# Kernel tuning notes

Measured on AMD Instinct MI355X. Metric: run time of the kernel, lower is better.

Reference implementation:

```python
import jax, jax.numpy as jnp
import numpy as np
import math

MODEL_DIM = 512
NUM_HEADS = 8
FFN_DIM = 2048
LN_EPS = 1e-5


def setup_inputs() -> dict:
    key = jax.random.key(0)
    ks = jax.random.split(key, 16)
    B, S, D, F = 1, 4096, MODEL_DIM, FFN_DIM
    s = 1.0 / math.sqrt(D)
    inp = {
        "x": jax.random.normal(ks[0], (B, S, D), dtype=jnp.float32),
        # Linear weights stored [in, out] (transpose of torch's [out, in]); y = x @ W + b
        "wq": jax.random.normal(ks[1], (D, D), dtype=jnp.float32) * s,
        "bq": jnp.zeros((D,), dtype=jnp.float32),
        "wk": jax.random.normal(ks[2], (D, D), dtype=jnp.float32) * s,
        "bk": jnp.zeros((D,), dtype=jnp.float32),
        "wv": jax.random.normal(ks[3], (D, D), dtype=jnp.float32) * s,
        "bv": jnp.zeros((D,), dtype=jnp.float32),
        "wo": jax.random.normal(ks[4], (D, D), dtype=jnp.float32) * s,
        "bo": jnp.zeros((D,), dtype=jnp.float32),
        "w1": jax.random.normal(ks[5], (D, F), dtype=jnp.float32) * s,
        "b1": jnp.zeros((F,), dtype=jnp.float32),
        "w2": jax.random.normal(ks[6], (F, D), dtype=jnp.float32) * (1.0 / math.sqrt(F)),
        "b2": jnp.zeros((D,), dtype=jnp.float32),
        "gamma": jnp.ones((D,), dtype=jnp.float32),
        "beta": jnp.zeros((D,), dtype=jnp.float32),
    }
    return inp


def _layer_norm(x, gamma, beta):
    mu = jnp.mean(x, axis=-1, keepdims=True)
    var = jnp.mean(jnp.square(x - mu), axis=-1, keepdims=True)
    return (x - mu) * jax.lax.rsqrt(var + LN_EPS) * gamma + beta


def reference(x, wq, bq, wk, bk, wv, bv, wo, bo, w1, b1, w2, b2, gamma, beta):
    B, S, D = x.shape
    H = NUM_HEADS
    dph = D // H
    q = x @ wq + bq
    k = x @ wk + bk
    v = x @ wv + bv
    # Faithful to original: direct view [B,S,D] -> [B*H, S, dph] (no head transpose)
    q = q.reshape(B * H, S, dph)
    k = k.reshape(B * H, S, dph)
    v = v.reshape(B * H, S, dph)
    scores = jnp.einsum('bqd,bkd->bqk', q, k) / math.sqrt(dph)  # [B*H, S, S]
    attn = jax.nn.softmax(scores, axis=-1)
    context = jnp.einsum('bqk,bkd->bqd', attn, v).reshape(B, S, D)
    attn_out = context @ wo + bo + x  # residual (dropout is identity in eval)
    ffn = jax.nn.relu(attn_out @ w1 + b1) @ w2 + b2
    out = _layer_norm(ffn + attn_out, gamma, beta)
    return out, attn
```

## Files before the change

### kernel.cpp

```cpp
#include <hip/hip_runtime.h>
#include <hip/hip_bf16.h>
#include <cstdint>
#include <cstddef>

#define SEQ 4096
#define DM  512
#define NH  8
#define DPH 64
#define FF  2048

using short8 = __attribute__((ext_vector_type(8))) short;
using f32x4  = __attribute__((ext_vector_type(4))) float;

__device__ inline float b2f(unsigned short u) {
    union { unsigned int i; float f; } c; c.i = ((unsigned int)u) << 16; return c.f;
}
__device__ inline unsigned short f2b(float f) {
    union { float f; unsigned int u; } c; c.f = f;
    unsigned int u = c.u;
    return (unsigned short)((u + 0x7fffu + ((u >> 16) & 1u)) >> 16);
}

template<int AF32>
__global__ __launch_bounds__(256) void gemm_kernel(
    const void* __restrict__ Av, const unsigned short* __restrict__ BT,
    const float* __restrict__ bias, const unsigned short* __restrict__ res,
    unsigned short* __restrict__ Cb, float* __restrict__ Cf,
    int M, int N, int K, long sA, long sB, long sC, float scale, int relu)
{
    const long z = blockIdx.z;
    BT += z * sB;
    const long co = z * sC;

    const int lane = threadIdx.x & 63;
    const int wid  = threadIdx.x >> 6;
    const int quad = lane >> 4;
    const int col  = lane & 15;
    const int m0 = blockIdx.y * 64 + wid * 16;
    const int n0 = blockIdx.x * 64;

    f32x4 acc[4];
    const f32x4 zero4 = {0.f, 0.f, 0.f, 0.f};
#pragma unroll
    for (int t = 0; t < 4; ++t) acc[t] = zero4;

    const unsigned short* arow16 = nullptr;
    const float*          arow32 = nullptr;
    if (AF32) arow32 = (const float*)Av          + z * sA + (size_t)(m0 + col) * K + quad * 8;
    else      arow16 = (const unsigned short*)Av + z * sA + (size_t)(m0 + col) * K + quad * 8;
    const unsigned short* brow = BT + (size_t)(n0 + col) * K + quad * 8;

    for (int k0 = 0; k0 < K; k0 += 32) {
        short8 a;
        if (AF32) {
            const float4 f0 = *(const float4*)(arow32 + k0);
            const float4 f1 = *(const float4*)(arow32 + k0 + 4);
            a[0] = (short)f2b(f0.x); a[1] = (short)f2b(f0.y);
            a[2] = (short)f2b(f0.z); a[3] = (short)f2b(f0.w);
            a[4] = (short)f2b(f1.x); a[5] = (short)f2b(f1.y);
            a[6] = (short)f2b(f1.z); a[7] = (short)f2b(f1.w);
        } else {
            a = *(const short8*)(arow16 + k0);
        }
#pragma unroll
        for (int t = 0; t < 4; ++t) {
            short8 b = *(const short8*)(brow + (size_t)t * 16 * K + k0);
            acc[t] = __builtin_amdgcn_mfma_f32_16x16x32_bf16(a, b, acc[t], 0, 0, 0);
        }
    }

#pragma unroll
    for (int t = 0; t < 4; ++t) {
        const int n = n0 + t * 16 + col;
        const float bv = bias ? bias[n] : 0.f;
#pragma unroll
        for (int r = 0; r < 4; ++r) {
            const int row = m0 + quad * 4 + r;
            float v = acc[t][r] * scale + bv;
            const size_t idx = (size_t)row * N + n;
            if (res)  v += b2f(res[idx]);
            if (relu) v = fmaxf(v, 0.f);
            if (Cf) Cf[co + idx] = v;
            else    Cb[co + idx] = f2b(v);
        }
    }
}

__global__ __launch_bounds__(256) void transpose_cast_kernel(
    const float* __restrict__ src, unsigned short* __restrict__ dst, int R, int C)
{
    __shared__ float tile[32][33];
    const int c0 = blockIdx.x * 32, r0 = blockIdx.y * 32;
    const int tx = threadIdx.x & 31, ty = threadIdx.x >> 5;
#pragma unroll
    for (int i = 0; i < 4; ++i)
        tile[ty + i * 8][tx] = src[(size_t)(r0 + ty + i * 8) * C + c0 + tx];
    __syncthreads();
#pragma unroll
    for (int i = 0; i < 4; ++i)
        dst[(size_t)(c0 + ty + i * 8) * R + r0 + tx] = f2b(tile[tx][ty + i * 8]);
}

__global__ __launch_bounds__(256) void transpose_kernel(
    const unsigned short* __restrict__ src, unsigned short* __restrict__ dst,
    int R, int C)
{
    __shared__ unsigned short tile[32][33];
    const long off = (long)blockIdx.z * (long)R * (long)C;
    src += off; dst += off;
    const int c0 = blockIdx.x * 32, r0 = blockIdx.y * 32;
    const int tx = threadIdx.x & 31, ty = threadIdx.x >> 5;
#pragma unroll
    for (int i = 0; i < 4; ++i)
        tile[ty + i * 8][tx] = src[(size_t)(r0 + ty + i * 8) * C + c0 + tx];
    __syncthreads();
#pragma unroll
    for (int i = 0; i < 4; ++i)
        dst[(size_t)(c0 + ty + i * 8) * R + r0 + tx] = tile[tx][ty + i * 8];
}

__global__ __launch_bounds__(256) void cast_kernel(
    const float* __restrict__ src, unsigned short* __restrict__ dst, int n4)
{
    const int i = blockIdx.x * 256 + threadIdx.x;
    if (i >= n4) return;
    const float4 v = ((const float4*)src)[i];
    union { unsigned short s[4]; unsigned long long u; } p;
    p.s[0] = f2b(v.x); p.s[1] = f2b(v.y); p.s[2] = f2b(v.z); p.s[3] = f2b(v.w);
    ((unsigned long long*)dst)[i] = p.u;
}

__global__ __launch_bounds__(256, 8) void fused_attn_kernel(
    const unsigned short* __restrict__ qb,
    const unsigned short* __restrict__ kb,
    const unsigned short* __restrict__ vT,
    float* __restrict__ att,
    unsigned short* __restrict__ ctx)
{
    __shared__ __align__(16) float Pl[4][16 * 36];
    __shared__ float smM[4][16];
    __shared__ float smS[4][16];
    __shared__ __align__(16) float cbuf[2][16 * 68];

    const int id    = blockIdx.x;
    const int h     = id & 7;
    const int strip = id >> 3;
    const int lane  = threadIdx.x & 63;
    const int w     = threadIdx.x >> 6;
    const int quad  = lane >> 4, col = lane & 15;
    const int m0    = strip * 16;

    const unsigned short* Qh = qb + (size_t)h * SEQ * DPH;
    const unsigned short* Kh = kb + (size_t)h * SEQ * DPH;
    const unsigned short* Vh = vT + (size_t)h * SEQ * DPH;
    float* atth = att + (size_t)h * SEQ * SEQ;
    unsigned short* ctxh = ctx + (size_t)h * SEQ * DPH;

    const unsigned short* qrow = Qh + (size_t)(m0 + col) * DPH + quad * 8;
    const short8 aq0 = *(const short8*)(qrow);
    const short8 aq1 = *(const short8*)(qrow + 32);

    const unsigned short* kbase = Kh + (size_t)(w * 1024 + col) * DPH + quad * 8;
    const float SC = 0.125f;
    const f32x4 zero4 = {0.f, 0.f, 0.f, 0.f};

    float m[4], s[4];
#pragma unroll
    for (int r = 0; r < 4; ++r) { m[r] = -1e30f; s[r] = 0.f; }

#pragma unroll 2
    for (int nt = 0; nt < 64; ++nt) {
        const unsigned short* kr = kbase + (size_t)nt * 16 * DPH;
        const short8 b0 = *(const short8*)(kr);
        const short8 b1 = *(const short8*)(kr + 32);
        f32x4 acc = zero4;
        acc = __builtin_amdgcn_mfma_f32_16x16x32_bf16(aq0, b0, acc, 0, 0, 0);
        acc = __builtin_amdgcn_mfma_f32_16x16x32_bf16(aq1, b1, acc, 0, 0, 0);
#pragma unroll
        for (int r = 0; r < 4; ++r) {
            const float v  = acc[r] * SC;
            const float nm = fmaxf(m[r], v);
            const float e  = __expf(fminf(m[r], v) - nm);
            s[r] = (v > m[r]) ? fmaf(s[r], e, 1.f) : (s[r] + e);
            m[r] = nm;
        }
    }
#pragma unroll
    for (int off = 1; off < 16; off <<= 1) {
#pragma unroll
        for (int r = 0; r < 4; ++r) {
            const float mo = __shfl_xor(m[r], off);
            const float so = __shfl_xor(s[r], off);
            const float nm = fmaxf(m[r], mo);
            s[r] = s[r] * __expf(m[r] - nm) + so * __expf(mo - nm);
            m[r] = nm;
        }
    }
    if (col == 0) {
#pragma unroll
        for (int r = 0; r < 4; ++r) { smM[w][quad * 4 + r] = m[r]; smS[w][quad * 4 + r] = s[r]; }
    }
    __syncthreads();
    float inv[4];
#pragma unroll
    for (int r = 0; r < 4; ++r) {
        const int row = quad * 4 + r;
        float M = smM[0][row], S = smS[0][row];
#pragma unroll
        for (int ww = 1; ww < 4; ++ww) {
            const float mo = smM[ww][row];
            const float so = smS[ww][row];
            const float nm = fmaxf(M, mo);
            S = S * __expf(M - nm) + so * __expf(mo - nm);
            M = nm;
        }
        m[r] = M;
        inv[r] = 1.f / S;
    }

    f32x4 cacc[4];
#pragma unroll
    for (int t = 0; t < 4; ++t) cacc[t] = zero4;

    float* Pw = Pl[w];
    float* abase = atth + (size_t)(m0 + quad * 4) * SEQ + w * 1024 + col;
    for (int pr = 0; pr < 32; ++pr) {
#pragma unroll
        for (int sub = 0; sub < 2; ++sub) {
            const int ntl = pr * 2 + sub;
            const unsigned short* kr = kbase + (size_t)ntl * 16 * DPH;
            const short8 b0 = *(const short8*)(kr);
            const short8 b1 = *(const short8*)(kr + 32);
            f32x4 acc = zero4;
            acc = __builtin_amdgcn_mfma_f32_16x16x32_bf16(aq0, b0, acc, 0, 0, 0);
            acc = __builtin_amdgcn_mfma_f32_16x16x32_bf16(aq1, b1, acc, 0, 0, 0);
            float* arow = abase + ntl * 16;
#pragma unroll
            for (int r = 0; r < 4; ++r) {
                const float p = __expf(fmaf(acc[r], SC, -m[r])) * inv[r];
                arow[(size_t)r * SEQ] = p;
                Pw[(quad * 4 + r) * 36 + sub * 16 + col] = p;
            }
        }
        const float4 pa0 = *(const float4*)(Pw + col * 36 + quad * 8);
        const float4 pa1 = *(const float4*)(Pw + col * 36 + quad * 8 + 4);
        union { unsigned short us[8]; short8 v; } ap;
        ap.us[0] = f2b(pa0.x); ap.us[1] = f2b(pa0.y);
        ap.us[2] = f2b(pa0.z); ap.us[3] = f2b(pa0.w);
        ap.us[4] = f2b(pa1.x); ap.us[5] = f2b(pa1.y);
        ap.us[6] = f2b(pa1.z); ap.us[7] = f2b(pa1.w);

        const int kg = w * 1024 + pr * 32;
        const unsigned short* vb0 = Vh + (size_t)col * SEQ + kg + quad * 8;
#pragma unroll
        for (int t = 0; t < 4; ++t) {
            const short8 bv = *(const short8*)(vb0 + (size_t)t * 16 * SEQ);
            cacc[t] = __builtin_amdgcn_mfma_f32_16x16x32_bf16(ap.v, bv, cacc[t], 0, 0, 0);
        }
    }

    if (w & 1) {
        float* cb = cbuf[w >> 1];
#pragma unroll
        for (int t = 0; t < 4; ++t)
#pragma unroll
            for (int r = 0; r < 4; ++r)
                cb[(quad * 4 + r) * 68 + t * 16 + col] = cacc[t][r];
    }
    __syncthreads();
    if (!(w & 1)) {
        const float* cb = cbuf[w >> 1];
#pragma unroll
        for (int t = 0; t < 4; ++t)
#pragma unroll
            for (int r = 0; r < 4; ++r)
                cacc[t][r] += cb[(quad * 4 + r) * 68 + t * 16 + col];
    }
    __syncthreads();
    if (w == 2) {
#pragma unroll
        for (int t = 0; t < 4; ++t)
#pragma unroll
            for (int r = 0; r < 4; ++r)
                cbuf[0][(quad * 4 + r) * 68 + t * 16 + col] = cacc[t][r];
    }
    __syncthreads();
    if (w == 0) {
#pragma unroll
        for (int t = 0; t < 4; ++t) {
#pragma unroll
            for (int r = 0; r < 4; ++r) {
                const float v = cacc[t][r] + cbuf[0][(quad * 4 + r) * 68 + t * 16 + col];
                ctxh[(size_t)(m0 + quad * 4 + r) * DPH + t * 16 + col] = f2b(v);
            }
        }
    }
}

__global__ __launch_bounds__(256) void ln_kernel(
    const float* __restrict__ pre,
    const float* __restrict__ gamma, const float* __restrict__ beta,
    float* __restrict__ out)
{
    __shared__ float redS[4], redQ[4];
    const float* p = pre + (size_t)blockIdx.x * 512;
    const int t = threadIdx.x;
    const int w = t >> 6, lane = t & 63;

    const float2 xv = *(const float2*)(p + t * 2);
    float s = xv.x + xv.y;
    float q = xv.x * xv.x + xv.y * xv.y;
#pragma unroll
    for (int off = 32; off; off >>= 1) {
        s += __shfl_xor(s, off);
        q += __shfl_xor(q, off);
    }
    if (lane == 0) { redS[w] = s; redQ[w] = q; }
    __syncthreads();
    s = redS[0] + redS[1] + redS[2] + redS[3];
    q = redQ[0] + redQ[1] + redQ[2] + redQ[3];

    const float mu  = s * (1.f / 512.f);
    const float var = q * (1.f / 512.f) - mu * mu;
    const float rs  = rsqrtf(var + 1e-5f);

    const size_t o = (size_t)blockIdx.x * 512 + t * 2;
    out[o]     = (xv.x - mu) * rs * gamma[t * 2]     + beta[t * 2];
    out[o + 1] = (xv.y - mu) * rs * gamma[t * 2 + 1] + beta[t * 2 + 1];
}

extern "C" void kernel_launch(void* const* d_in, const int* in_sizes, int n_in,
                              void* d_out, int out_size, void* d_ws, size_t ws_size,
                              hipStream_t stream)
{
    (void)in_sizes; (void)n_in; (void)out_size; (void)ws_size;

    const float* x     = (const float*)d_in[0];
    const float* wq    = (const float*)d_in[1];
    const float* bq    = (const float*)d_in[2];
    const float* wk    = (const float*)d_in[3];
    const float* bk    = (const float*)d_in[4];
    const float* wv    = (const float*)d_in[5];
    const float* bv    = (const float*)d_in[6];
    const float* wo    = (const float*)d_in[7];
    const float* bo    = (const float*)d_in[8];
    const float* w1    = (const float*)d_in[9];
    const float* b1    = (const float*)d_in[10];
    const float* w2    = (const float*)d_in[11];
    const float* b2    = (const float*)d_in[12];
    const float* gamma = (const float*)d_in[13];
    const float* beta  = (const float*)d_in[14];

    float* out = (float*)d_out;
    float* att = out + (size_t)SEQ * DM;

    char* wsp = (char*)d_ws;
    auto alloc = [&](size_t bytes) {
        char* p = wsp;
        wsp += (bytes + 255) & ~(size_t)255;
        return p;
    };
    unsigned short* wqT  = (unsigned short*)alloc((size_t)DM * DM * 2);
    unsigned short* wkT  = (unsigned short*)alloc((size_t)DM * DM * 2);
    unsigned short* wvT  = (unsigned short*)alloc((size_t)DM * DM * 2);
    unsigned short* woT  = (unsigned short*)alloc((size_t)DM * DM * 2);
    unsigned short* w1T  = (unsigned short*)alloc((size_t)DM * FF * 2);
    unsigned short* w2T  = (unsigned short*)alloc((size_t)FF * DM * 2);
    unsigned short* xb   = (unsigned short*)alloc((size_t)SEQ * DM * 2);
    unsigned short* qb   = (unsigned short*)alloc((size_t)SEQ * DM * 2);
    unsigned short* kb   = (unsigned short*)alloc((size_t)SEQ * DM * 2);
    unsigned short* vb   = (unsigned short*)alloc((size_t)SEQ * DM * 2);
    unsigned short* vT   = (unsigned short*)alloc((size_t)SEQ * DM * 2);
    unsigned short* ctx  = (unsigned short*)alloc((size_t)SEQ * DM * 2);
    unsigned short* aout = (unsigned short*)alloc((size_t)SEQ * DM * 2);
    unsigned short* ffn1 = (unsigned short*)alloc((size_t)SEQ * FF * 2);
    float*          pre  = (float*)alloc((size_t)SEQ * DM * 4);

    const dim3 blk(256);

    cast_kernel<<<dim3((SEQ * DM / 4 + 255) / 256), blk, 0, stream>>>(x, xb, SEQ * DM / 4);

    transpose_cast_kernel<<<dim3(16, 16), blk, 0, stream>>>(wq, wqT, DM, DM);
    transpose_cast_kernel<<<dim3(16, 16), blk, 0, stream>>>(wk, wkT, DM, DM);
    transpose_cast_kernel<<<dim3(16, 16), blk, 0, stream>>>(wv, wvT, DM, DM);
    transpose_cast_kernel<<<dim3(16, 16), blk, 0, stream>>>(wo, woT, DM, DM);
    transpose_cast_kernel<<<dim3(64, 16), blk, 0, stream>>>(w1, w1T, DM, FF);
    transpose_cast_kernel<<<dim3(16, 64), blk, 0, stream>>>(w2, w2T, FF, DM);

    gemm_kernel<0><<<dim3(8, 64, 1), blk, 0, stream>>>(xb, wqT, bq, nullptr, qb, nullptr,
                                                       SEQ, DM, DM, 0, 0, 0, 1.f, 0);
    gemm_kernel<0><<<dim3(8, 64, 1), blk, 0, stream>>>(xb, wkT, bk, nullptr, kb, nullptr,
                                                       SEQ, DM, DM, 0, 0, 0, 1.f, 0);
    gemm_kernel<0><<<dim3(8, 64, 1), blk, 0, stream>>>(xb, wvT, bv, nullptr, vb, nullptr,
                                                       SEQ, DM, DM, 0, 0, 0, 1.f, 0);

    transpose_kernel<<<dim3(2, 128, 8), blk, 0, stream>>>(vb, vT, SEQ, DPH);

    fused_attn_kernel<<<dim3(2048), blk, 0, stream>>>(qb, kb, vT, att, ctx);

    gemm_kernel<0><<<dim3(8, 64, 1), blk, 0, stream>>>(ctx, woT, bo, xb, aout, nullptr,
                                                       SEQ, DM, DM, 0, 0, 0, 1.f, 0);

    gemm_kernel<0><<<dim3(32, 64, 1), blk, 0, stream>>>(aout, w1T, b1, nullptr, ffn1, nullptr,
                                                        SEQ, FF, DM, 0, 0, 0, 1.f, 1);

    gemm_kernel<0><<<dim3(8, 64, 1), blk, 0, stream>>>(ffn1, w2T, b2, aout, nullptr, pre,
                                                       SEQ, DM, FF, 0, 0, 0, 1.f, 0);

    ln_kernel<<<dim3(SEQ), blk, 0, stream>>>(pre, gamma, beta, out);
}
```

Before: 1.165 ms.

## Tile GEMMs through shared memory and coalesce attention-probability stores

Replaces the register-only GEMM, where each wave streamed A and B straight from global memory, with an LDS-tiled kernel. It uses 128xBN block tiles, register prefetch of the next K slice, and 4xNI MFMA sub-tiles per wave, which raises operand reuse. In the attention kernel, the probability matrix is now written to global memory as float4 row chunks read back from the existing LDS staging buffer, instead of scattered scalar column stores. This adds LDS traffic and two barriers per K step, and the larger tiles halve the GEMM grid sizes.

```diff
diff --git a/kernel.cpp b/kernel.cpp
--- a/kernel.cpp
+++ b/kernel.cpp
@@ -21,67 +21,91 @@
     return (unsigned short)((u + 0x7fffu + ((u >> 16) & 1u)) >> 16);
 }
 
-template<int AF32>
-__global__ __launch_bounds__(256) void gemm_kernel(
-    const void* __restrict__ Av, const unsigned short* __restrict__ BT,
+template<int BN, int NI>
+__global__ __launch_bounds__(256) void tgemm_kernel(
+    const unsigned short* __restrict__ A, const unsigned short* __restrict__ BT,
     const float* __restrict__ bias, const unsigned short* __restrict__ res,
     unsigned short* __restrict__ Cb, float* __restrict__ Cf,
-    int M, int N, int K, long sA, long sB, long sC, float scale, int relu)
-{
-    const long z = blockIdx.z;
-    BT += z * sB;
-    const long co = z * sC;
-
-    const int lane = threadIdx.x & 63;
-    const int wid  = threadIdx.x >> 6;
-    const int quad = lane >> 4;
-    const int col  = lane & 15;
-    const int m0 = blockIdx.y * 64 + wid * 16;
-    const int n0 = blockIdx.x * 64;
-
-    f32x4 acc[4];
+    int M, int N, int K, int relu)
+{
+    __shared__ __align__(16) unsigned short As[128 * 40];
+    __shared__ __align__(16) unsigned short Bs[BN * 40];
+
+    const int t    = threadIdx.x;
+    const int lane = t & 63;
+    const int wid  = t >> 6;
+    const int wr   = wid >> 1, wc = wid & 1;
+    const int quad = lane >> 4, cl = lane & 15;
+    const int m0 = blockIdx.y * 128;
+    const int n0 = blockIdx.x * BN;
+
+    const int srow = t >> 2;
+    const int skc  = t & 3;
+
+    const unsigned short* Arow0 = A  + (size_t)(m0 + srow) * K + skc * 8;
+    const unsigned short* Arow1 = Arow0 + (size_t)64 * K;
+    const unsigned short* Brow0 = BT + (size_t)(n0 + srow) * K + skc * 8;
+    const unsigned short* Brow1 = Brow0 + (size_t)64 * K;
+
+    f32x4 acc[4][NI];
     const f32x4 zero4 = {0.f, 0.f, 0.f, 0.f};
 #pragma unroll
-    for (int t = 0; t < 4; ++t) acc[t] = zero4;
-
-    const unsigned short* arow16 = nullptr;
-    const float*          arow32 = nullptr;
-    if (AF32) arow32 = (const float*)Av          + z * sA + (size_t)(m0 + col) * K + quad * 8;
-    else      arow16 = (const unsigned short*)Av + z * sA + (size_t)(m0 + col) * K + quad * 8;
-    const unsigned short* brow = BT + (size_t)(n0 + col) * K + quad * 8;
+    for (int mi = 0; mi < 4; ++mi)
+#pragma unroll
+        for (int ni = 0; ni < NI; ++ni) acc[mi][ni] = zero4;
+
+    short8 ar0, ar1, br0, br1;
+    ar0 = *(const short8*)(Arow0);
+    ar1 = *(const short8*)(Arow1);
+    br0 = *(const short8*)(Brow0);
+    if constexpr (NI == 4) br1 = *(const short8*)(Brow1);
 
     for (int k0 = 0; k0 < K; k0 += 32) {
-        short8 a;
-        if (AF32) {
-            const float4 f0 = *(const float4*)(arow32 + k0);
-            const float4 f1 = *(const float4*)(arow32 + k0 + 4);
-            a[0] = (short)f2b(f0.x); a[1] = (short)f2b(f0.y);
-            a[2] = (short)f2b(f0.z); a[3] = (short)f2b(f0.w);
-            a[4] = (short)f2b(f1.x); a[5] = (short)f2b(f1.y);
-            a[6] = (short)f2b(f1.z); a[7] = (short)f2b(f1.w);
-        } else {
-            a = *(const short8*)(arow16 + k0);
-        }
-#pragma unroll
-        for (int t = 0; t < 4; ++t) {
-            short8 b = *(const short8*)(brow + (size_t)t * 16 * K + k0);
-            acc[t] = __builtin_amdgcn_mfma_f32_16x16x32_bf16(a, b, acc[t], 0, 0, 0);
-        }
-    }
-
-#pragma unroll
-    for (int t = 0; t < 4; ++t) {
-        const int n = n0 + t * 16 + col;
+        __syncthreads();
+        *(short8*)(&As[srow * 40 + skc * 8])        = ar0;
+        *(short8*)(&As[(srow + 64) * 40 + skc * 8]) = ar1;
+        *(short8*)(&Bs[srow * 40 + skc * 8])        = br0;
+        if constexpr (NI == 4) *(short8*)(&Bs[(srow + 64) * 40 + skc * 8]) = br1;
+        __syncthreads();
+
+        const int kn = k0 + 32;
+        if (kn < K) {
+            ar0 = *(const short8*)(Arow0 + kn);
+            ar1 = *(const short8*)(Arow1 + kn);
+            br0 = *(const short8*)(Brow0 + kn);
+            if constexpr (NI == 4) br1 = *(const short8*)(Brow1 + kn);
+        }
+
+        short8 af[4], bf[NI];
+#pragma unroll
+        for (int mi = 0; mi < 4; ++mi)
+            af[mi] = *(const short8*)(&As[(wr * 64 + mi * 16 + cl) * 40 + quad * 8]);
+#pragma unroll
+        for (int ni = 0; ni < NI; ++ni)
+            bf[ni] = *(const short8*)(&Bs[(wc * (BN / 2) + ni * 16 + cl) * 40 + quad * 8]);
+#pragma unroll
+        for (int mi = 0; mi < 4; ++mi)
+#pragma unroll
+            for (int ni = 0; ni < NI; ++ni)
+                acc[mi][ni] = __builtin_amdgcn_mfma_f32_16x16x32_bf16(af[mi], bf[ni], acc[mi][ni], 0, 0, 0);
+    }
+
+#pragma unroll
+    for (int ni = 0; ni < NI; ++ni) {
+        const int n = n0 + wc * (BN / 2) + ni * 16 + cl;
         const float bv = bias ? bias[n] : 0.f;
 #pragma unroll
-        for (int r = 0; r < 4; ++r) {
-            const int row = m0 + quad * 4 + r;
-            float v = acc[t][r] * scale + bv;
-            const size_t idx = (size_t)row * N + n;
-            if (res)  v += b2f(res[idx]);
-            if (relu) v = fmaxf(v, 0.f);
-            if (Cf) Cf[co + idx] = v;
-            else    Cb[co + idx] = f2b(v);
+        for (int mi = 0; mi < 4; ++mi) {
+#pragma unroll
+            for (int r = 0; r < 4; ++r) {
+                const int row = m0 + wr * 64 + mi * 16 + quad * 4 + r;
+                float v = acc[mi][ni][r] + bv;
+                const size_t idx = (size_t)row * N + n;
+                if (res)  v += b2f(res[idx]);
+                if (relu) v = fmaxf(v, 0.f);
+                if (Cf) Cf[idx] = v;
+                else    Cb[idx] = f2b(v);
+            }
         }
     }
 }
@@ -223,7 +247,9 @@
     for (int t = 0; t < 4; ++t) cacc[t] = zero4;
 
     float* Pw = Pl[w];
-    float* abase = atth + (size_t)(m0 + quad * 4) * SEQ + w * 1024 + col;
+    float* abase = atth + (size_t)m0 * SEQ + w * 1024;
+    const int srow2  = lane >> 3;
+    const int schunk = lane & 7;
     for (int pr = 0; pr < 32; ++pr) {
 #pragma unroll
         for (int sub = 0; sub < 2; ++sub) {
@@ -234,13 +260,17 @@
             f32x4 acc = zero4;
             acc = __builtin_amdgcn_mfma_f32_16x16x32_bf16(aq0, b0, acc, 0, 0, 0);
             acc = __builtin_amdgcn_mfma_f32_16x16x32_bf16(aq1, b1, acc, 0, 0, 0);
-            float* arow = abase + ntl * 16;
 #pragma unroll
             for (int r = 0; r < 4; ++r) {
                 const float p = __expf(fmaf(acc[r], SC, -m[r])) * inv[r];
-                arow[(size_t)r * SEQ] = p;
                 Pw[(quad * 4 + r) * 36 + sub * 16 + col] = p;
             }
+        }
+#pragma unroll
+        for (int sset = 0; sset < 2; ++sset) {
+            const int prow = srow2 + sset * 8;
+            const float4 pv = *(const float4*)(Pw + prow * 36 + schunk * 4);
+            *(float4*)(abase + (size_t)prow * SEQ + pr * 32 + schunk * 4) = pv;
         }
         const float4 pa0 = *(const float4*)(Pw + col * 36 + quad * 8);
         const float4 pa1 = *(const float4*)(Pw + col * 36 + quad * 8 + 4);
@@ -387,25 +417,25 @@
     transpose_cast_kernel<<<dim3(64, 16), blk, 0, stream>>>(w1, w1T, DM, FF);
     transpose_cast_kernel<<<dim3(16, 64), blk, 0, stream>>>(w2, w2T, FF, DM);
 
-    gemm_kernel<0><<<dim3(8, 64, 1), blk, 0, stream>>>(xb, wqT, bq, nullptr, qb, nullptr,
-                                                       SEQ, DM, DM, 0, 0, 0, 1.f, 0);
-    gemm_kernel<0><<<dim3(8, 64, 1), blk, 0, stream>>>(xb, wkT, bk, nullptr, kb, nullptr,
-                                                       SEQ, DM, DM, 0, 0, 0, 1.f, 0);
-    gemm_kernel<0><<<dim3(8, 64, 1), blk, 0, stream>>>(xb, wvT, bv, nullptr, vb, nullptr,
-                                                       SEQ, DM, DM, 0, 0, 0, 1.f, 0);
+    tgemm_kernel<64, 2><<<dim3(8, 32), blk, 0, stream>>>(xb, wqT, bq, nullptr, qb, nullptr,
+                                                         SEQ, DM, DM, 0);
+    tgemm_kernel<64, 2><<<dim3(8, 32), blk, 0, stream>>>(xb, wkT, bk, nullptr, kb, nullptr,
+                                                         SEQ, DM, DM, 0);
+    tgemm_kernel<64, 2><<<dim3(8, 32), blk, 0, stream>>>(xb, wvT, bv, nullptr, vb, nullptr,
+                                                         SEQ, DM, DM, 0);
 
     transpose_kernel<<<dim3(2, 128, 8), blk, 0, stream>>>(vb, vT, SEQ, DPH);
 
     fused_attn_kernel<<<dim3(2048), blk, 0, stream>>>(qb, kb, vT, att, ctx);
 
-    gemm_kernel<0><<<dim3(8, 64, 1), blk, 0, stream>>>(ctx, woT, bo, xb, aout, nullptr,
-                                                       SEQ, DM, DM, 0, 0, 0, 1.f, 0);
-
-    gemm_kernel<0><<<dim3(32, 64, 1), blk, 0, stream>>>(aout, w1T, b1, nullptr, ffn1, nullptr,
-                                                        SEQ, FF, DM, 0, 0, 0, 1.f, 1);
-
-    gemm_kernel<0><<<dim3(8, 64, 1), blk, 0, stream>>>(ffn1, w2T, b2, aout, nullptr, pre,
-                                                       SEQ, DM, FF, 0, 0, 0, 1.f, 0);
+    tgemm_kernel<64, 2><<<dim3(8, 32), blk, 0, stream>>>(ctx, woT, bo, xb, aout, nullptr,
+                                                         SEQ, DM, DM, 0);
+
+    tgemm_kernel<128, 4><<<dim3(16, 32), blk, 0, stream>>>(aout, w1T, b1, nullptr, ffn1, nullptr,
+                                                           SEQ, FF, DM, 1);
+
+    tgemm_kernel<64, 2><<<dim3(8, 32), blk, 0, stream>>>(ffn1, w2T, b2, aout, nullptr, pre,
+                                                         SEQ, DM, FF, 0);
 
     ln_kernel<<<dim3(SEQ), blk, 0, stream>>>(pre, gamma, beta, out);
 }
```

New measurement: 982.5 us. 1.19x faster.
